# Performance work log

Hardware: AMD Instinct MI355X
Metric: run time of the kernel (lower is better)

Reference implementation:

```python
import jax, jax.numpy as jnp
import numpy as np

N = 8192  # number of observations (rows of configuration)
D = 128   # embedding dimension


def _pair_indices(n):
    """Pair ordering of the original TF loop: for upper in 2..n-1, lower in 0..upper-1.
    (Pair (0,1) is never emitted by the original code.)"""
    counts = np.arange(2, n, dtype=np.int64)          # block u contributes u pairs
    uppers = np.repeat(counts, counts)
    starts = np.concatenate([np.zeros(1, np.int64), np.cumsum(counts)[:-1]])
    lowers = np.arange(uppers.shape[0], dtype=np.int64) - np.repeat(starts, counts)
    return lowers.astype(np.int32), uppers.astype(np.int32)


def setup_inputs() -> dict:
    key = jax.random.key(0)
    inputs = jax.random.normal(key, (N, D), dtype=jnp.float32)
    return {"inputs": inputs}


def reference(inputs):
    n = inputs.shape[0]
    lowers, uppers = _pair_indices(n)  # static (numpy) index arrays
    # trace(X^T (e_l-e_u)(e_l-e_u)^T X) == ||x_l - x_u||^2
    # Gram trick: ||x_l - x_u||^2 = ||x_l||^2 + ||x_u||^2 - 2 <x_l, x_u>
    sq = jnp.sum(inputs * inputs, axis=1)          # [n]
    gram = inputs @ inputs.T                        # [n, n]
    dists = sq[lowers] + sq[uppers] - 2.0 * gram[lowers, uppers]
    # Original TensorArray has size (n^2-n)/2 but only (n^2-n)/2 - 1 slots are
    # written (pair (0,1) is skipped); the last slot stacks as zero.
    out = jnp.concatenate([dists, jnp.zeros((1,), dists.dtype)])
    return out[None, :]  # tf.expand_dims(..., 0)
```

## Files before the change

kernel.cpp:

```cpp
#include <hip/hip_runtime.h>
#include <hip/hip_bf16.h>

#define NROWS 8192
#define DIM   128
#define NT    64
#define NBLK  (NT * (NT + 1) / 2)
#define TOTAL_OUT 33550336u

typedef short bf16x8 __attribute__((ext_vector_type(8)));
typedef float f32x4  __attribute__((ext_vector_type(4)));
typedef unsigned short u16x8 __attribute__((ext_vector_type(8)));

static __device__ inline unsigned short f32_to_bf16(float f) {
    unsigned int u = __float_as_uint(f);
    u += 0x7FFFu + ((u >> 16) & 1u);
    return (unsigned short)(u >> 16);
}

__global__ __launch_bounds__(64) void prep_kernel(const float* __restrict__ X,
                                                  unsigned short* __restrict__ Xb,
                                                  float* __restrict__ sq,
                                                  float* __restrict__ out) {
    const int row  = blockIdx.x;
    const int lane = threadIdx.x;
    const float2 v = *reinterpret_cast<const float2*>(X + (size_t)row * DIM + lane * 2);
    unsigned int packed = ((unsigned int)f32_to_bf16(v.y) << 16) | f32_to_bf16(v.x);
    *reinterpret_cast<unsigned int*>(Xb + (size_t)row * DIM + lane * 2) = packed;
    float s = v.x * v.x + v.y * v.y;
    #pragma unroll
    for (int o = 32; o > 0; o >>= 1) s += __shfl_xor(s, o);
    if (lane == 0) sq[row] = s;
    if (row == 0 && lane == 0) out[TOTAL_OUT - 1] = 0.0f;
}

__global__ __launch_bounds__(256, 2) void pdist_kernel(const unsigned short* __restrict__ Xb,
                                                       const float* __restrict__ sq,
                                                       float* __restrict__ out) {
    __shared__ char smem[65536];
    char* ldsA = smem;
    char* ldsB = smem + 32768;

    const int t  = threadIdx.x;
    const int bt = blockIdx.x;
    int bj = (int)((sqrtf(8.0f * (float)bt + 1.0f) - 1.0f) * 0.5f);
    while ((bj + 1) * (bj + 2) / 2 <= bt) ++bj;
    while (bj * (bj + 1) / 2 > bt) --bj;
    const int bi = bt - bj * (bj + 1) / 2;

    const unsigned short* srcA = Xb + (size_t)bi * 128 * DIM;
    const unsigned short* srcB = Xb + (size_t)bj * 128 * DIM;
    #pragma unroll
    for (int i = 0; i < 8; ++i) {
        int chunk = t + i * 256;
        int row   = chunk >> 4;
        int c     = chunk & 15;
        int sc    = c ^ (row & 7);
        *reinterpret_cast<u16x8*>(ldsA + row * 256 + sc * 16) =
            *reinterpret_cast<const u16x8*>(srcA + row * DIM + c * 8);
        *reinterpret_cast<u16x8*>(ldsB + row * 256 + sc * 16) =
            *reinterpret_cast<const u16x8*>(srcB + row * DIM + c * 8);
    }
    __syncthreads();

    const int wid  = t >> 6;
    const int lane = t & 63;
    const int wr   = wid >> 1;
    const int wc   = wid & 1;
    const int lrow = lane & 15;
    const int kgrp = lane >> 4;

    f32x4 acc[4][4];
    const f32x4 fzero = {0.f, 0.f, 0.f, 0.f};
    #pragma unroll
    for (int m = 0; m < 4; ++m)
        #pragma unroll
        for (int n = 0; n < 4; ++n) acc[m][n] = fzero;

    #pragma unroll
    for (int kk = 0; kk < 4; ++kk) {
        const int chunk = kk * 4 + kgrp;
        bf16x8 a[4], b[4];
        #pragma unroll
        for (int m = 0; m < 4; ++m) {
            int row = wr * 64 + m * 16 + lrow;
            a[m] = *reinterpret_cast<const bf16x8*>(ldsA + row * 256 + (chunk ^ (row & 7)) * 16);
        }
        #pragma unroll
        for (int n = 0; n < 4; ++n) {
            int row = wc * 64 + n * 16 + lrow;
            b[n] = *reinterpret_cast<const bf16x8*>(ldsB + row * 256 + (chunk ^ (row & 7)) * 16);
        }
        #pragma unroll
        for (int m = 0; m < 4; ++m)
            #pragma unroll
            for (int n = 0; n < 4; ++n)
                acc[m][n] = __builtin_amdgcn_mfma_f32_16x16x32_bf16(a[m], b[n], acc[m][n], 0, 0, 0);
    }

    const int l0 = bi * 128 + wr * 64;
    const int u0 = bj * 128 + wc * 64;
    const int rj = kgrp * 4;

    float squ[4];
    f32x4 sql[4];
    #pragma unroll
    for (int n = 0; n < 4; ++n) squ[n] = sq[u0 + n * 16 + lrow];
    #pragma unroll
    for (int m = 0; m < 4; ++m)
        sql[m] = *reinterpret_cast<const f32x4*>(sq + l0 + m * 16 + rj);

    if (bi != bj) {
        #pragma unroll
        for (int m = 0; m < 4; ++m) {
            #pragma unroll
            for (int n = 0; n < 4; ++n) {
                const int u = u0 + n * 16 + lrow;
                const size_t base = ((size_t)u * (u - 1)) / 2 - 1 + (size_t)(l0 + m * 16 + rj);
                f32x4 d;
                #pragma unroll
                for (int j = 0; j < 4; ++j) d[j] = sql[m][j] + squ[n] - 2.0f * acc[m][n][j];
                __builtin_memcpy(out + base, &d, 16);
            }
        }
    } else {
        #pragma unroll
        for (int m = 0; m < 4; ++m) {
            #pragma unroll
            for (int n = 0; n < 4; ++n) {
                const int u = u0 + n * 16 + lrow;
                #pragma unroll
                for (int j = 0; j < 4; ++j) {
                    const int l = l0 + m * 16 + rj + j;
                    if (l < u && u >= 2) {
                        out[((size_t)u * (u - 1)) / 2 - 1 + l] = sql[m][j] + squ[n] - 2.0f * acc[m][n][j];
                    }
                }
            }
        }
    }
}

extern "C" void kernel_launch(void* const* d_in, const int* in_sizes, int n_in,
                              void* d_out, int out_size, void* d_ws, size_t ws_size,
                              hipStream_t stream) {
    const float* X = (const float*)d_in[0];
    float* out = (float*)d_out;
    unsigned short* Xb = (unsigned short*)d_ws;
    float* sq = (float*)((char*)d_ws + (size_t)NROWS * DIM * 2);

    prep_kernel<<<NROWS, 64, 0, stream>>>(X, Xb, sq, out);
    pdist_kernel<<<NBLK, 256, 0, stream>>>(Xb, sq, out);
}
```

Baseline: 52.59 us.

## Pre-swizzle bf16 operands into MFMA fragment order and load directly from global

The prep kernel now writes the bf16 copy of X in the exact per-lane MFMA fragment order (16-row groups by k-chunk by lane), so the pairwise kernel can fetch A/B fragments straight from global/L2 with double-buffered register prefetch instead of staging 64 KB through LDS. Dropping the LDS allocation and the barrier lets the launch bound request three blocks per CU. Output stores become nontemporal to keep the large write stream from polluting cache. The cost is redundant global fragment reads across waves that previously shared LDS tiles, plus higher register pressure from the double buffers.

```diff
diff --git a/kernel.cpp b/kernel.cpp
--- a/kernel.cpp
+++ b/kernel.cpp
@@ -10,6 +10,7 @@
 typedef short bf16x8 __attribute__((ext_vector_type(8)));
 typedef float f32x4  __attribute__((ext_vector_type(4)));
 typedef unsigned short u16x8 __attribute__((ext_vector_type(8)));
+typedef f32x4 f32x4_a4 __attribute__((aligned(4)));
 
 static __device__ inline unsigned short f32_to_bf16(float f) {
     unsigned int u = __float_as_uint(f);
@@ -17,50 +18,49 @@
     return (unsigned short)(u >> 16);
 }
 
-__global__ __launch_bounds__(64) void prep_kernel(const float* __restrict__ X,
-                                                  unsigned short* __restrict__ Xb,
-                                                  float* __restrict__ sq,
-                                                  float* __restrict__ out) {
-    const int row  = blockIdx.x;
-    const int lane = threadIdx.x;
-    const float2 v = *reinterpret_cast<const float2*>(X + (size_t)row * DIM + lane * 2);
-    unsigned int packed = ((unsigned int)f32_to_bf16(v.y) << 16) | f32_to_bf16(v.x);
-    *reinterpret_cast<unsigned int*>(Xb + (size_t)row * DIM + lane * 2) = packed;
-    float s = v.x * v.x + v.y * v.y;
-    #pragma unroll
-    for (int o = 32; o > 0; o >>= 1) s += __shfl_xor(s, o);
-    if (lane == 0) sq[row] = s;
-    if (row == 0 && lane == 0) out[TOTAL_OUT - 1] = 0.0f;
+__global__ __launch_bounds__(256) void prep_kernel(const float* __restrict__ X,
+                                                   unsigned short* __restrict__ Xr,
+                                                   float* __restrict__ sq,
+                                                   float* __restrict__ out) {
+    __shared__ float sm[16][17];
+    const int g = blockIdx.x;
+    const int t = threadIdx.x;
+    const int kk = t >> 6, lane = t & 63;
+    const int lrow = lane & 15, kgrp = lane >> 4;
+
+    const float* src = X + (size_t)(g * 16 + lrow) * DIM + (kk * 4 + kgrp) * 8;
+    const float4 v0 = *reinterpret_cast<const float4*>(src);
+    const float4 v1 = *reinterpret_cast<const float4*>(src + 4);
+
+    u16x8 h;
+    h[0] = f32_to_bf16(v0.x); h[1] = f32_to_bf16(v0.y);
+    h[2] = f32_to_bf16(v0.z); h[3] = f32_to_bf16(v0.w);
+    h[4] = f32_to_bf16(v1.x); h[5] = f32_to_bf16(v1.y);
+    h[6] = f32_to_bf16(v1.z); h[7] = f32_to_bf16(v1.w);
+    *reinterpret_cast<u16x8*>(Xr + ((size_t)(g * 4 + kk) * 64 + lane) * 8) = h;
+
+    float p = v0.x * v0.x + v0.y * v0.y + v0.z * v0.z + v0.w * v0.w
+            + v1.x * v1.x + v1.y * v1.y + v1.z * v1.z + v1.w * v1.w;
+    sm[lrow][kk * 4 + kgrp] = p;
+    __syncthreads();
+    if (t < 16) {
+        float s = 0.f;
+        #pragma unroll
+        for (int j = 0; j < 16; ++j) s += sm[t][j];
+        sq[g * 16 + t] = s;
+    }
+    if (g == 0 && t == 0) out[TOTAL_OUT - 1] = 0.0f;
 }
 
-__global__ __launch_bounds__(256, 2) void pdist_kernel(const unsigned short* __restrict__ Xb,
+__global__ __launch_bounds__(256, 3) void pdist_kernel(const unsigned short* __restrict__ Xr,
                                                        const float* __restrict__ sq,
                                                        float* __restrict__ out) {
-    __shared__ char smem[65536];
-    char* ldsA = smem;
-    char* ldsB = smem + 32768;
-
     const int t  = threadIdx.x;
     const int bt = blockIdx.x;
     int bj = (int)((sqrtf(8.0f * (float)bt + 1.0f) - 1.0f) * 0.5f);
     while ((bj + 1) * (bj + 2) / 2 <= bt) ++bj;
     while (bj * (bj + 1) / 2 > bt) --bj;
     const int bi = bt - bj * (bj + 1) / 2;
-
-    const unsigned short* srcA = Xb + (size_t)bi * 128 * DIM;
-    const unsigned short* srcB = Xb + (size_t)bj * 128 * DIM;
-    #pragma unroll
-    for (int i = 0; i < 8; ++i) {
-        int chunk = t + i * 256;
-        int row   = chunk >> 4;
-        int c     = chunk & 15;
-        int sc    = c ^ (row & 7);
-        *reinterpret_cast<u16x8*>(ldsA + row * 256 + sc * 16) =
-            *reinterpret_cast<const u16x8*>(srcA + row * DIM + c * 8);
-        *reinterpret_cast<u16x8*>(ldsB + row * 256 + sc * 16) =
-            *reinterpret_cast<const u16x8*>(srcB + row * DIM + c * 8);
-    }
-    __syncthreads();
 
     const int wid  = t >> 6;
     const int lane = t & 63;
@@ -69,6 +69,10 @@
     const int lrow = lane & 15;
     const int kgrp = lane >> 4;
 
+    const bf16x8* __restrict__ F = reinterpret_cast<const bf16x8*>(Xr);
+    const int gA = bi * 8 + wr * 4;
+    const int gB = bj * 8 + wc * 4;
+
     f32x4 acc[4][4];
     const f32x4 fzero = {0.f, 0.f, 0.f, 0.f};
     #pragma unroll
@@ -76,25 +80,27 @@
         #pragma unroll
         for (int n = 0; n < 4; ++n) acc[m][n] = fzero;
 
+    bf16x8 a[2][4], b[2][4];
+    #pragma unroll
+    for (int m = 0; m < 4; ++m) {
+        a[0][m] = F[((gA + m) * 4 + 0) * 64 + lane];
+        b[0][m] = F[((gB + m) * 4 + 0) * 64 + lane];
+    }
     #pragma unroll
     for (int kk = 0; kk < 4; ++kk) {
-        const int chunk = kk * 4 + kgrp;
-        bf16x8 a[4], b[4];
-        #pragma unroll
-        for (int m = 0; m < 4; ++m) {
-            int row = wr * 64 + m * 16 + lrow;
-            a[m] = *reinterpret_cast<const bf16x8*>(ldsA + row * 256 + (chunk ^ (row & 7)) * 16);
-        }
-        #pragma unroll
-        for (int n = 0; n < 4; ++n) {
-            int row = wc * 64 + n * 16 + lrow;
-            b[n] = *reinterpret_cast<const bf16x8*>(ldsB + row * 256 + (chunk ^ (row & 7)) * 16);
+        const int cur = kk & 1, nxt = cur ^ 1;
+        if (kk < 3) {
+            #pragma unroll
+            for (int m = 0; m < 4; ++m) {
+                a[nxt][m] = F[((gA + m) * 4 + kk + 1) * 64 + lane];
+                b[nxt][m] = F[((gB + m) * 4 + kk + 1) * 64 + lane];
+            }
         }
         #pragma unroll
         for (int m = 0; m < 4; ++m)
             #pragma unroll
             for (int n = 0; n < 4; ++n)
-                acc[m][n] = __builtin_amdgcn_mfma_f32_16x16x32_bf16(a[m], b[n], acc[m][n], 0, 0, 0);
+                acc[m][n] = __builtin_amdgcn_mfma_f32_16x16x32_bf16(a[cur][m], b[cur][n], acc[m][n], 0, 0, 0);
     }
 
     const int l0 = bi * 128 + wr * 64;
@@ -119,7 +125,7 @@
                 f32x4 d;
                 #pragma unroll
                 for (int j = 0; j < 4; ++j) d[j] = sql[m][j] + squ[n] - 2.0f * acc[m][n][j];
-                __builtin_memcpy(out + base, &d, 16);
+                __builtin_nontemporal_store(d, reinterpret_cast<f32x4_a4*>(out + base));
             }
         }
     } else {
@@ -132,7 +138,8 @@
                 for (int j = 0; j < 4; ++j) {
                     const int l = l0 + m * 16 + rj + j;
                     if (l < u && u >= 2) {
-                        out[((size_t)u * (u - 1)) / 2 - 1 + l] = sql[m][j] + squ[n] - 2.0f * acc[m][n][j];
+                        const float d = sql[m][j] + squ[n] - 2.0f * acc[m][n][j];
+                        __builtin_nontemporal_store(d, out + ((size_t)u * (u - 1)) / 2 - 1 + l);
                     }
                 }
             }
@@ -145,9 +152,9 @@
                               hipStream_t stream) {
     const float* X = (const float*)d_in[0];
     float* out = (float*)d_out;
-    unsigned short* Xb = (unsigned short*)d_ws;
+    unsigned short* Xr = (unsigned short*)d_ws;
     float* sq = (float*)((char*)d_ws + (size_t)NROWS * DIM * 2);
 
-    prep_kernel<<<NROWS, 64, 0, stream>>>(X, Xb, sq, out);
-    pdist_kernel<<<NBLK, 256, 0, stream>>>(Xb, sq, out);
+    prep_kernel<<<NROWS / 16, 256, 0, stream>>>(X, Xr, sq, out);
+    pdist_kernel<<<NBLK, 256, 0, stream>>>(Xr, sq, out);
 }
```

Result: slower. 149.9 us (+185.0%).
